# Optimization experiments

Hardware: AMD Instinct MI355X
Metric: run time of the kernel (lower is better)

Reference implementation:

```python
import jax, jax.numpy as jnp
import numpy as np

D_MODEL = 1024
N_HEADS = 16
D_K = D_MODEL // N_HEADS
B, T = 4, 2048


def setup_inputs() -> dict:
    key = jax.random.key(0)
    ks = jax.random.split(key, 6)
    scale = 1.0 / np.sqrt(D_MODEL)
    q = jax.random.normal(ks[0], (B, T, D_MODEL), dtype=jnp.float32)
    # causal mask: True = masked / ignored (upper triangle)
    causal = jnp.triu(jnp.ones((T, T), dtype=bool), k=1)
    mask = jnp.broadcast_to(causal, (B, 1, T, T))
    Wq = jax.random.normal(ks[1], (D_MODEL, D_MODEL), dtype=jnp.float32) * scale
    Wk = jax.random.normal(ks[2], (D_MODEL, D_MODEL), dtype=jnp.float32) * scale
    Wv = jax.random.normal(ks[3], (D_MODEL, D_MODEL), dtype=jnp.float32) * scale
    Wo = jax.random.normal(ks[4], (D_MODEL, D_MODEL), dtype=jnp.float32) * scale
    bq = jnp.zeros((D_MODEL,), jnp.float32)
    bk = jnp.zeros((D_MODEL,), jnp.float32)
    bv = jnp.zeros((D_MODEL,), jnp.float32)
    bo = jnp.zeros((D_MODEL,), jnp.float32)
    return {"q": q, "mask": mask, "Wq": Wq, "bq": bq, "Wk": Wk, "bk": bk,
            "Wv": Wv, "bv": bv, "Wo": Wo, "bo": bo}


def reference(q, mask, Wq, bq, Wk, bk, Wv, bv, Wo, bo):
    # Self-attention: k = v = q (module defaults). Weights stored torch-style
    # (out, in): y = x @ W.T + b.
    b, tq, _ = q.shape
    qh = (q @ Wq.T + bq).reshape(b, tq, N_HEADS, D_K).transpose(0, 2, 1, 3)  # (B,H,T,dk)
    kh = (q @ Wk.T + bk).reshape(b, tq, N_HEADS, D_K).transpose(0, 2, 1, 3)
    vh = (q @ Wv.T + bv).reshape(b, tq, N_HEADS, D_K).transpose(0, 2, 1, 3)
    attn = jnp.einsum('bhqd,bhkd->bhqk', qh, kh) / np.sqrt(D_K).astype(np.float32)
    attn = jnp.where(mask, -jnp.inf, attn)
    attn = jax.nn.softmax(attn, axis=-1)
    out = jnp.einsum('bhqk,bhkd->bhqd', attn, vh)
    out = out.transpose(0, 2, 1, 3).reshape(b, tq, D_MODEL)
    return out @ Wo.T + bo
```

## Files before the change

kernel.cpp:

```cpp
#include <hip/hip_runtime.h>
#include <hip/hip_bf16.h>
#include <stdint.h>

#define D_MODEL 1024
#define NH      16
#define DKH     64
#define BATCH   4
#define SEQ     2048
#define MROWS   (BATCH*SEQ)

typedef __hip_bfloat16 bf16;
typedef __attribute__((ext_vector_type(8))) short  bf16x8;
typedef __attribute__((ext_vector_type(4))) short  bf16x4;
typedef __attribute__((ext_vector_type(4))) float  f32x4;
typedef __attribute__((ext_vector_type(4))) int    i32x4;
typedef __attribute__((ext_vector_type(2))) unsigned int u32x2;

#define CEXP 0.18033688011112042f

__device__ __forceinline__ bf16 f2bf(float x){ return __float2bfloat16(x); }

__device__ __forceinline__ void gload_lds16(const void* g, void* l) {
  __builtin_amdgcn_global_load_lds(
      (const __attribute__((address_space(1))) unsigned int*)g,
      (__attribute__((address_space(3))) unsigned int*)l, 16, 0, 0);
}

__device__ __forceinline__ unsigned int pack2bf(float a, float b) {
  return __builtin_amdgcn_perm(__float_as_uint(b) + 0x8000u,
                               __float_as_uint(a) + 0x8000u, 0x07060302u);
}

__global__ __launch_bounds__(256)
void cvt_all(const float* __restrict__ q,
             const float* __restrict__ w0, const float* __restrict__ w1,
             const float* __restrict__ w2, const float* __restrict__ w3,
             bf16* __restrict__ qdst, bf16* __restrict__ wdst)
{
  const int NQB = (MROWS * D_MODEL) / 1024;
  const int bid = blockIdx.x;
  const float* src;
  bf16* dst;
  int i;
  if (bid < NQB) {
    src = q; dst = qdst;
    i = bid * 1024 + threadIdx.x * 4;
  } else {
    const int b2 = bid - NQB;
    const int w = b2 >> 10;
    src = (w == 0) ? w0 : (w == 1) ? w1 : (w == 2) ? w2 : w3;
    dst = wdst + (size_t)w * (D_MODEL * D_MODEL);
    i = (b2 & 1023) * 1024 + threadIdx.x * 4;
  }
  f32x4 v = *(const f32x4*)&src[i];
  union { bf16 e[4]; bf16x4 v4; } u;
  u.e[0] = f2bf(v[0]); u.e[1] = f2bf(v[1]);
  u.e[2] = f2bf(v[2]); u.e[3] = f2bf(v[3]);
  *(bf16x4*)&dst[i] = u.v4;
}

template <typename TO>
__global__ __launch_bounds__(256)
void gemm_bt_bias(const bf16* __restrict__ A, const bf16* __restrict__ Wbase,
                  const float* __restrict__ b0, const float* __restrict__ b1,
                  const float* __restrict__ b2, TO* __restrict__ Cbase,
                  float scale0)
{
  __shared__ __align__(16) short lA[128 * 64];
  __shared__ __align__(16) short lB[128 * 64];

  const int z = blockIdx.z;
  const bf16* Bt = Wbase + (size_t)z * (D_MODEL * D_MODEL);
  const float* bias = (z == 0) ? b0 : (z == 1) ? b1 : b2;
  TO* C = Cbase + (size_t)z * ((size_t)MROWS * D_MODEL);
  const float sc = (z == 0) ? scale0 : 1.0f;
  const int K = D_MODEL, N = D_MODEL;

  const int tid  = threadIdx.x;
  const int lane = tid & 63;
  const int wave = tid >> 6;
  const int lm   = lane & 15;
  const int quad = lane >> 4;
  const int wm   = (wave & 1) * 64;
  const int wn   = (wave >> 1) * 64;
  const int bm   = blockIdx.x * 128;
  const int bn   = blockIdx.y * 128;

  f32x4 acc[4][4] = {};

  const int rr   = tid >> 3;
  const int kofs = ((tid & 7) ^ (rr & 7)) * 8;
  const bf16* pa[4]; const bf16* pb[4];
#pragma unroll
  for (int p = 0; p < 4; ++p) {
    pa[p] = A  + (int64_t)(bm + rr + 32 * p) * K + kofs;
    pb[p] = Bt + (int64_t)(bn + rr + 32 * p) * K + kofs;
  }

  for (int k0 = 0; k0 < K; k0 += 64) {
    __syncthreads();
#pragma unroll
    for (int p = 0; p < 4; ++p) {
      gload_lds16(pa[p] + k0, &lA[(tid + p * 256) * 8]);
      gload_lds16(pb[p] + k0, &lB[(tid + p * 256) * 8]);
    }
    __syncthreads();

#pragma unroll
    for (int kk = 0; kk < 2; ++kk) {
      bf16x8 af[4], bfr[4];
#pragma unroll
      for (int i = 0; i < 4; ++i) {
        const int ra = wm + i * 16 + lm;
        af[i]  = *(const bf16x8*)&lA[ra * 64 + (((kk * 4 + quad) ^ (ra & 7))) * 8];
        const int rb = wn + i * 16 + lm;
        bfr[i] = *(const bf16x8*)&lB[rb * 64 + (((kk * 4 + quad) ^ (rb & 7))) * 8];
      }
#pragma unroll
      for (int i = 0; i < 4; ++i)
#pragma unroll
        for (int j = 0; j < 4; ++j)
          acc[i][j] = __builtin_amdgcn_mfma_f32_16x16x32_bf16(af[i], bfr[j], acc[i][j], 0, 0, 0);
    }
  }

  if constexpr (sizeof(TO) == 2) {
    if (z == 2) {
      bf16* Vt = (bf16*)C;
#pragma unroll
      for (int j = 0; j < 4; ++j) {
        const int n = bn + wn + j * 16 + lm;
        const float bv = bias[n];
#pragma unroll
        for (int i = 0; i < 4; ++i) {
          const int m0 = bm + wm + i * 16 + quad * 4;
          const int64_t base = (int64_t)((m0 >> 11) * 16 + (n >> 6)) * (DKH * SEQ)
                             + (n & 63) * SEQ + (m0 & 2047);
          union { bf16 e[4]; bf16x4 v4; } u;
#pragma unroll
          for (int r = 0; r < 4; ++r) u.e[r] = f2bf(acc[i][j][r] + bv);
          *(bf16x4*)&Vt[base] = u.v4;
        }
      }
      return;
    }
  }

#pragma unroll
  for (int j = 0; j < 4; ++j) {
    const int n = bn + wn + j * 16 + lm;
    const float bv = bias[n];
#pragma unroll
    for (int i = 0; i < 4; ++i) {
#pragma unroll
      for (int r = 0; r < 4; ++r) {
        const int m = bm + wm + i * 16 + quad * 4 + r;
        const float v = (acc[i][j][r] + bv) * sc;
        if constexpr (sizeof(TO) == 2) C[(int64_t)m * N + n] = f2bf(v);
        else                           C[(int64_t)m * N + n] = v;
      }
    }
  }
}

__global__ __launch_bounds__(256)
void attn_causal(const bf16* __restrict__ Q, const bf16* __restrict__ Kg,
                 const bf16* __restrict__ Vt, bf16* __restrict__ O)
{
  __shared__ __align__(16) short lK[2][64 * 64];
  __shared__ __align__(16) short lV[2][64 * 64];
  __shared__ __align__(16) short lP[4 * 16 * 64];

  const int bid  = blockIdx.x;
  const int qt   = 31 - (bid >> 6);
  const int bh   = bid & 63;

  const int tid  = threadIdx.x;
  const int lane = tid & 63;
  const int wave = tid >> 6;
  const int lm   = lane & 15;
  const int quad = lane >> 4;
  const int qbase = qt * 64;
  const int64_t qkbase = (int64_t)((bh >> 4) * SEQ) * D_MODEL + (bh & 15) * DKH;
  const bf16* Kbase = Kg + qkbase;
  const bf16* Vbase = Vt + (int64_t)bh * DKH * SEQ;

  bf16x8 qf[2];
  {
    const bf16* qrow = Q + qkbase + (int64_t)(qbase + wave * 16 + lm) * D_MODEL;
    qf[0] = *(const bf16x8*)&qrow[quad * 8];
    qf[1] = *(const bf16x8*)&qrow[32 + quad * 8];
  }

  f32x4 o_acc[4] = {};
  float lsum = 0.f;

  const int srow = tid >> 3;
  const int sg   = (tid & 7) ^ (srow & 7);
  short* pw = &lP[wave * 1024];
  const int wqv = wave * 16 + lm;

  const bf16* kp0 = Kbase + (int64_t)srow        * D_MODEL + sg * 8;
  const bf16* kp1 = Kbase + (int64_t)(srow + 32) * D_MODEL + sg * 8;
  const bf16* vp0 = Vbase + (int64_t)srow        * SEQ + sg * 8;
  const bf16* vp1 = Vbase + (int64_t)(srow + 32) * SEQ + sg * 8;

#define STAGE(KB, BUF)                                                        \
  do {                                                                        \
    gload_lds16(kp0 + (int64_t)(KB) * D_MODEL, &lK[BUF][tid * 8]);            \
    gload_lds16(kp1 + (int64_t)(KB) * D_MODEL, &lK[BUF][(tid + 256) * 8]);    \
    gload_lds16(vp0 + (KB), &lV[BUF][tid * 8]);                               \
    gload_lds16(vp1 + (KB), &lV[BUF][(tid + 256) * 8]);                       \
  } while (0)

  STAGE(0, 0);

  for (int kt = 0; kt <= qt; ++kt) {
    const int cur = kt & 1;
    __syncthreads();
    if (kt < qt) STAGE((kt + 1) * 64, cur ^ 1);

    const short* lKc = lK[cur];
    const short* lVc = lV[cur];

    f32x4 s[4];
#pragma unroll
    for (int ni = 0; ni < 4; ++ni) {
      const int row = ni * 16 + lm;
      f32x4 zz = {};
      bf16x8 k0 = *(const bf16x8*)&lKc[row * 64 + ((quad       ^ (row & 7))) * 8];
      bf16x8 k1 = *(const bf16x8*)&lKc[row * 64 + (((4 + quad) ^ (row & 7))) * 8];
      zz = __builtin_amdgcn_mfma_f32_16x16x32_bf16(k0, qf[0], zz, 0, 0, 0);
      zz = __builtin_amdgcn_mfma_f32_16x16x32_bf16(k1, qf[1], zz, 0, 0, 0);
      s[ni] = zz;
    }

    if (kt == qt) {
#pragma unroll
      for (int ni = 0; ni < 4; ++ni) {
        const int kp = ni * 16 + quad * 4;
#pragma unroll
        for (int r = 0; r < 4; ++r)
          if (kp + r > wqv) s[ni][r] = -1e30f;
      }
    }

#pragma unroll
    for (int ni = 0; ni < 4; ++ni) {
      const float p0 = __builtin_amdgcn_exp2f(s[ni][0]);
      const float p1 = __builtin_amdgcn_exp2f(s[ni][1]);
      const float p2 = __builtin_amdgcn_exp2f(s[ni][2]);
      const float p3 = __builtin_amdgcn_exp2f(s[ni][3]);
      lsum += (p0 + p1) + (p2 + p3);
      u32x2 pk;
      pk[0] = pack2bf(p0, p1);
      pk[1] = pack2bf(p2, p3);
      *(u32x2*)&pw[lm * 64 + (((ni * 4 + quad) ^ lm)) * 4] = pk;
    }

#pragma unroll
    for (int kk = 0; kk < 2; ++kk) {
      const int h0 = (kk * 8 + 2 * quad) ^ lm;
      union { bf16x8 v; u32x2 h[2]; } pu;
      pu.h[0] = *(const u32x2*)&pw[lm * 64 + h0 * 4];
      pu.h[1] = *(const u32x2*)&pw[lm * 64 + (h0 ^ 1) * 4];
#pragma unroll
      for (int di = 0; di < 4; ++di) {
        const int vrow = di * 16 + lm;
        bf16x8 vb = *(const bf16x8*)&lVc[vrow * 64 + (((kk * 4 + quad) ^ (vrow & 7))) * 8];
        o_acc[di] = __builtin_amdgcn_mfma_f32_16x16x32_bf16(pu.v, vb, o_acc[di], 0, 0, 0);
      }
    }
  }
#undef STAGE

  lsum += __shfl_xor(lsum, 16);
  lsum += __shfl_xor(lsum, 32);
  const float linv = 1.0f / lsum;
  float lr[4];
#pragma unroll
  for (int r = 0; r < 4; ++r) lr[r] = __shfl(linv, quad * 4 + r);

#pragma unroll
  for (int di = 0; di < 4; ++di)
#pragma unroll
    for (int r = 0; r < 4; ++r) {
      const int qrow = qbase + wave * 16 + quad * 4 + r;
      O[qkbase + (int64_t)qrow * D_MODEL + di * 16 + lm] = f2bf(o_acc[di][r] * lr[r]);
    }
}

extern "C" void kernel_launch(void* const* d_in, const int* in_sizes, int n_in,
                              void* d_out, int out_size, void* d_ws, size_t ws_size,
                              hipStream_t stream)
{
  const float* q  = (const float*)d_in[0];
  const float* Wq = (const float*)d_in[2];
  const float* bq = (const float*)d_in[3];
  const float* Wk = (const float*)d_in[4];
  const float* bk = (const float*)d_in[5];
  const float* Wv = (const float*)d_in[6];
  const float* bv = (const float*)d_in[7];
  const float* Wo = (const float*)d_in[8];
  const float* bo = (const float*)d_in[9];
  float* out = (float*)d_out;

  const size_t NQ = (size_t)MROWS * D_MODEL;
  const size_t NW = (size_t)D_MODEL * D_MODEL;

  bf16* qb  = (bf16*)d_ws;
  bf16* Wb  = qb + NQ;
  bf16* Qw  = Wb + 4 * NW;
  bf16* Kw  = Qw + NQ;
  bf16* Vtw = Kw + NQ;

  cvt_all<<<dim3(NQ / 1024 + 4 * NW / 1024), 256, 0, stream>>>(
      q, Wq, Wk, Wv, Wo, qb, Wb);

  gemm_bt_bias<bf16><<<dim3(MROWS / 128, D_MODEL / 128, 3), 256, 0, stream>>>(
      qb, Wb, bq, bk, bv, Qw, CEXP);

  attn_causal<<<dim3(BATCH * NH * (SEQ / 64)), 256, 0, stream>>>(Qw, Kw, Vtw, qb);

  gemm_bt_bias<float><<<dim3(MROWS / 128, D_MODEL / 128, 1), 256, 0, stream>>>(
      qb, Wb + 3 * NW, bo, bo, bo, out, 1.0f);
}
```

Measured before the change: 288.8 us.

## Replace GEMMs with 512-thread 128x256 tiles and triple-buffered async LDS pipeline

Both projection GEMMs now use a new kernel with 512 threads and 128x256 output tiles. It keeps a three-slot LDS ring filled by direct global-to-LDS loads issued two k-steps ahead, and replaces the double __syncthreads per step with a vmcnt wait plus one barrier. The QKV projections are fused into one N=3072 launch, and MFMA sections are raised in priority with s_setprio. This aims to hide global-load latency and raise arithmetic intensity per block. In exchange it uses much more LDS per block (about 144KB), which limits occupancy, and produces fewer blocks for the output projection.

```diff
diff --git a/kernel.cpp b/kernel.cpp
--- a/kernel.cpp
+++ b/kernel.cpp
@@ -13,7 +13,6 @@
 typedef __attribute__((ext_vector_type(8))) short  bf16x8;
 typedef __attribute__((ext_vector_type(4))) short  bf16x4;
 typedef __attribute__((ext_vector_type(4))) float  f32x4;
-typedef __attribute__((ext_vector_type(4))) int    i32x4;
 typedef __attribute__((ext_vector_type(2))) unsigned int u32x2;
 
 #define CEXP 0.18033688011112042f
@@ -59,62 +58,75 @@
   *(bf16x4*)&dst[i] = u.v4;
 }
 
-template <typename TO>
-__global__ __launch_bounds__(256)
-void gemm_bt_bias(const bf16* __restrict__ A, const bf16* __restrict__ Wbase,
-                  const float* __restrict__ b0, const float* __restrict__ b1,
-                  const float* __restrict__ b2, TO* __restrict__ Cbase,
-                  float scale0)
+template <int MODE>
+__global__ __launch_bounds__(512, 2)
+void gemm8(const bf16* __restrict__ A, const bf16* __restrict__ W,
+           const float* __restrict__ b0, const float* __restrict__ b1,
+           const float* __restrict__ b2, void* __restrict__ Cbase)
 {
-  __shared__ __align__(16) short lA[128 * 64];
-  __shared__ __align__(16) short lB[128 * 64];
-
-  const int z = blockIdx.z;
-  const bf16* Bt = Wbase + (size_t)z * (D_MODEL * D_MODEL);
-  const float* bias = (z == 0) ? b0 : (z == 1) ? b1 : b2;
-  TO* C = Cbase + (size_t)z * ((size_t)MROWS * D_MODEL);
-  const float sc = (z == 0) ? scale0 : 1.0f;
-  const int K = D_MODEL, N = D_MODEL;
+  constexpr int K    = D_MODEL;
+  constexpr int NT   = K / 64;
+  constexpr int SLOT = (128 + 256) * 64;
+  __shared__ __align__(16) short ring[3 * SLOT];
 
   const int tid  = threadIdx.x;
   const int lane = tid & 63;
   const int wave = tid >> 6;
   const int lm   = lane & 15;
   const int quad = lane >> 4;
-  const int wm   = (wave & 1) * 64;
-  const int wn   = (wave >> 1) * 64;
+  const int wm   = (wave >> 2) * 64;
+  const int wn   = (wave & 3) * 64;
   const int bm   = blockIdx.x * 128;
-  const int bn   = blockIdx.y * 128;
+  const int bn   = blockIdx.y * 256;
+
+  const int rr    = tid >> 3;
+  const int kperm = ((tid & 7) ^ (rr & 7)) * 8;
+  const bf16* aS0 = A + (int64_t)(bm + rr) * K + kperm;
+  const bf16* aS1 = aS0 + (int64_t)64 * K;
+  const bf16* bS0 = W + (int64_t)(bn + rr) * K + kperm;
+  const bf16* bS1 = bS0 + (int64_t)64 * K;
+  const bf16* bS2 = bS0 + (int64_t)128 * K;
+  const bf16* bS3 = bS0 + (int64_t)192 * K;
 
   f32x4 acc[4][4] = {};
 
-  const int rr   = tid >> 3;
-  const int kofs = ((tid & 7) ^ (rr & 7)) * 8;
-  const bf16* pa[4]; const bf16* pb[4];
-#pragma unroll
-  for (int p = 0; p < 4; ++p) {
-    pa[p] = A  + (int64_t)(bm + rr + 32 * p) * K + kofs;
-    pb[p] = Bt + (int64_t)(bn + rr + 32 * p) * K + kofs;
-  }
-
-  for (int k0 = 0; k0 < K; k0 += 64) {
-    __syncthreads();
-#pragma unroll
-    for (int p = 0; p < 4; ++p) {
-      gload_lds16(pa[p] + k0, &lA[(tid + p * 256) * 8]);
-      gload_lds16(pb[p] + k0, &lB[(tid + p * 256) * 8]);
-    }
-    __syncthreads();
-
+#define STAGE8(T, S)                                                          \
+  do {                                                                        \
+    const int k0_ = (T) * 64;                                                 \
+    short* As_ = &ring[(S) * SLOT];                                           \
+    short* Bs_ = As_ + 128 * 64;                                              \
+    gload_lds16(aS0 + k0_, &As_[tid * 8]);                                    \
+    gload_lds16(aS1 + k0_, &As_[(tid + 512) * 8]);                            \
+    gload_lds16(bS0 + k0_, &Bs_[tid * 8]);                                    \
+    gload_lds16(bS1 + k0_, &Bs_[(tid + 512) * 8]);                            \
+    gload_lds16(bS2 + k0_, &Bs_[(tid + 1024) * 8]);                           \
+    gload_lds16(bS3 + k0_, &Bs_[(tid + 1536) * 8]);                           \
+  } while (0)
+
+  STAGE8(0, 0);
+  STAGE8(1, 1);
+
+#pragma unroll
+  for (int t = 0; t < NT; ++t) {
+    if (t < NT - 1) asm volatile("s_waitcnt vmcnt(6)" ::: "memory");
+    else            asm volatile("s_waitcnt vmcnt(0)" ::: "memory");
+    __builtin_amdgcn_s_barrier();
+    asm volatile("" ::: "memory");
+    if (t + 2 < NT) STAGE8(t + 2, (t + 2) % 3);
+
+    const short* As = &ring[(t % 3) * SLOT];
+    const short* Bs = As + 128 * 64;
+
+    __builtin_amdgcn_s_setprio(1);
 #pragma unroll
     for (int kk = 0; kk < 2; ++kk) {
       bf16x8 af[4], bfr[4];
 #pragma unroll
       for (int i = 0; i < 4; ++i) {
         const int ra = wm + i * 16 + lm;
-        af[i]  = *(const bf16x8*)&lA[ra * 64 + (((kk * 4 + quad) ^ (ra & 7))) * 8];
+        af[i]  = *(const bf16x8*)&As[ra * 64 + (((kk * 4 + quad) ^ (ra & 7))) * 8];
         const int rb = wn + i * 16 + lm;
-        bfr[i] = *(const bf16x8*)&lB[rb * 64 + (((kk * 4 + quad) ^ (rb & 7))) * 8];
+        bfr[i] = *(const bf16x8*)&Bs[rb * 64 + (((kk * 4 + quad) ^ (rb & 7))) * 8];
       }
 #pragma unroll
       for (int i = 0; i < 4; ++i)
@@ -122,42 +134,59 @@
         for (int j = 0; j < 4; ++j)
           acc[i][j] = __builtin_amdgcn_mfma_f32_16x16x32_bf16(af[i], bfr[j], acc[i][j], 0, 0, 0);
     }
-  }
-
-  if constexpr (sizeof(TO) == 2) {
-    if (z == 2) {
-      bf16* Vt = (bf16*)C;
+    __builtin_amdgcn_s_setprio(0);
+  }
+#undef STAGE8
+
+  if constexpr (MODE == 1) {
+    float* Cp = (float*)Cbase;
+#pragma unroll
+    for (int j = 0; j < 4; ++j) {
+      const int n = bn + wn + j * 16 + lm;
+      const float bv = b0[n];
+#pragma unroll
+      for (int i = 0; i < 4; ++i)
+#pragma unroll
+        for (int r = 0; r < 4; ++r) {
+          const int m = bm + wm + i * 16 + quad * 4 + r;
+          Cp[(int64_t)m * D_MODEL + n] = acc[i][j][r] + bv;
+        }
+    }
+  } else {
+    const int proj = bn >> 10;
+    const int nl0  = bn & 1023;
+    const float* bias = (proj == 0) ? b0 : (proj == 1) ? b1 : b2;
+    if (proj == 2) {
+      bf16* Vt = (bf16*)Cbase + 2 * (size_t)MROWS * D_MODEL;
 #pragma unroll
       for (int j = 0; j < 4; ++j) {
-        const int n = bn + wn + j * 16 + lm;
-        const float bv = bias[n];
+        const int nl = nl0 + wn + j * 16 + lm;
+        const float bv = bias[nl];
 #pragma unroll
         for (int i = 0; i < 4; ++i) {
           const int m0 = bm + wm + i * 16 + quad * 4;
-          const int64_t base = (int64_t)((m0 >> 11) * 16 + (n >> 6)) * (DKH * SEQ)
-                             + (n & 63) * SEQ + (m0 & 2047);
+          const int64_t base = (int64_t)((m0 >> 11) * 16 + (nl >> 6)) * (DKH * SEQ)
+                             + (nl & 63) * SEQ + (m0 & 2047);
           union { bf16 e[4]; bf16x4 v4; } u;
 #pragma unroll
           for (int r = 0; r < 4; ++r) u.e[r] = f2bf(acc[i][j][r] + bv);
           *(bf16x4*)&Vt[base] = u.v4;
         }
       }
-      return;
-    }
-  }
-
-#pragma unroll
-  for (int j = 0; j < 4; ++j) {
-    const int n = bn + wn + j * 16 + lm;
-    const float bv = bias[n];
-#pragma unroll
-    for (int i = 0; i < 4; ++i) {
-#pragma unroll
-      for (int r = 0; r < 4; ++r) {
-        const int m = bm + wm + i * 16 + quad * 4 + r;
-        const float v = (acc[i][j][r] + bv) * sc;
-        if constexpr (sizeof(TO) == 2) C[(int64_t)m * N + n] = f2bf(v);
-        else                           C[(int64_t)m * N + n] = v;
+    } else {
+      bf16* Cp = (bf16*)Cbase + (size_t)proj * MROWS * D_MODEL;
+      const float sc = (proj == 0) ? CEXP : 1.0f;
+#pragma unroll
+      for (int j = 0; j < 4; ++j) {
+        const int nl = nl0 + wn + j * 16 + lm;
+        const float bv = bias[nl];
+#pragma unroll
+        for (int i = 0; i < 4; ++i)
+#pragma unroll
+          for (int r = 0; r < 4; ++r) {
+            const int m = bm + wm + i * 16 + quad * 4 + r;
+            Cp[(int64_t)m * D_MODEL + nl] = f2bf((acc[i][j][r] + bv) * sc);
+          }
       }
     }
   }
@@ -317,11 +346,11 @@
   cvt_all<<<dim3(NQ / 1024 + 4 * NW / 1024), 256, 0, stream>>>(
       q, Wq, Wk, Wv, Wo, qb, Wb);
 
-  gemm_bt_bias<bf16><<<dim3(MROWS / 128, D_MODEL / 128, 3), 256, 0, stream>>>(
-      qb, Wb, bq, bk, bv, Qw, CEXP);
+  gemm8<0><<<dim3(MROWS / 128, 3 * D_MODEL / 256), 512, 0, stream>>>(
+      qb, Wb, bq, bk, bv, Qw);
 
   attn_causal<<<dim3(BATCH * NH * (SEQ / 64)), 256, 0, stream>>>(Qw, Kw, Vtw, qb);
 
-  gemm_bt_bias<float><<<dim3(MROWS / 128, D_MODEL / 128, 1), 256, 0, stream>>>(
-      qb, Wb + 3 * NW, bo, bo, bo, out, 1.0f);
-}
+  gemm8<1><<<dim3(MROWS / 128, D_MODEL / 256), 512, 0, stream>>>(
+      qb, Wb + 3 * NW, bo, bo, bo, out);
+}
```

Result: faster. 278.6 us (-3.6%).
